# Performance work log

Hardware: AMD Instinct MI355X
Metric: run time of the kernel (lower is better)

The kernel has to match this reference:

```python
import jax, jax.numpy as jnp
import numpy as np

WINDOW = 128  # crop size (compute_crops default window_size)


def centre_crop(centroids, window_size, h, w):
    # centroids: [C,2] int; returns flat gather coords [2, C*ws*ws]
    half = window_size // 2
    cy = jnp.clip(centroids[:, 0], half, h - half)
    cx = jnp.clip(centroids[:, 1], half, w - half)
    gy, gx = jnp.meshgrid(jnp.arange(window_size), jnp.arange(window_size), indexing='ij')
    rows = (cy - half)[:, None, None] + gy[None]  # [C,ws,ws]
    cols = (cx - half)[:, None, None] + gx[None]
    return jnp.stack([rows.reshape(-1), cols.reshape(-1)])  # [2, C*ws*ws]


def setup_inputs() -> dict:
    key = jax.random.key(0)
    ks = jax.random.split(key, 8)
    E, S, C, H, W = 6, 1, 512, 1024, 1024
    Dh = 16
    return {
        'x': jax.random.normal(ks[0], (E, H, W), dtype=jnp.float32),
        'sigma': jax.random.uniform(ks[1], (S, H, W), dtype=jnp.float32),
        'c': jax.random.normal(ks[2], (C, E), dtype=jnp.float32),
        'W1': jax.random.normal(ks[3], (E + S, Dh), dtype=jnp.float32) * 0.3,
        'b1': jnp.zeros((Dh,), dtype=jnp.float32),
        'W2': jax.random.normal(ks[4], (Dh, Dh), dtype=jnp.float32) * 0.3,
        'b2': jnp.zeros((Dh,), dtype=jnp.float32),
        'W3': jax.random.normal(ks[5], (Dh, 1), dtype=jnp.float32) * 0.3,
        'b3': jnp.zeros((1,), dtype=jnp.float32),
        'centroids_idx': jax.random.randint(ks[6], (C, 2), 0, H, dtype=jnp.int32),
    }


def reference(x, sigma, c, W1, b1, W2, b2, W3, b3, centroids_idx):
    E, h, w = x.shape
    S = sigma.shape[0]
    C = c.shape[0]
    ws = WINDOW
    mesh = centre_crop(centroids_idx, ws, h, w)  # [2, C*ws*ws]
    # gather per-instance windows from concatenated embedding+sigma maps
    xs = jnp.concatenate([x, sigma], axis=0)  # [E+S, H, W]
    g = xs[:, mesh[0], mesh[1]]               # [E+S, C*ws*ws]
    g = g.reshape(E + S, C, ws, ws).transpose(1, 0, 2, 3)  # [C, E+S, ws, ws]
    # subtract centroid descriptor from embedding channels (feature_engineering '0')
    g = jnp.concatenate([g[:, :E] - c[:, :, None, None], g[:, E:]], axis=1)
    feats = g.transpose(0, 2, 3, 1).reshape(-1, E + S)  # [(C*ws*ws), E+S]
    # per-pixel probability MLP (ProbabilityNet)
    hdn = jax.nn.relu(feats @ W1 + b1)
    hdn = jax.nn.relu(hdn @ W2 + b2)
    prob = jax.nn.sigmoid(hdn @ W3 + b3)
    prob = prob.reshape(C, 1, ws, ws)
    # instance-id / coordinate table for the downstream scatter (iidd)
    inst = jnp.repeat(jnp.arange(C, dtype=mesh.dtype), ws * ws)
    iidd = jnp.concatenate([inst[None], mesh], axis=0)  # [3, C*ws*ws]
    return prob, iidd
```

## Files before the change

### kernel.cpp

```cpp
#include <hip/hip_runtime.h>

#define HW (1024 * 1024)
#define PLANE 8388608

typedef _Float16 half4 __attribute__((ext_vector_type(4)));
typedef _Float16 half8 __attribute__((ext_vector_type(8)));
typedef float floatx4 __attribute__((ext_vector_type(4)));


__global__ __launch_bounds__(512) void build_worklist(
    const int* __restrict__ cent, int* __restrict__ ws)
{
    __shared__ int cnt[8];
    if (threadIdx.x < 8) cnt[threadIdx.x] = 0;
    __syncthreads();
    for (int t = threadIdx.x; t < 4096; t += 512) {
        const int w = t >> 3, g = t & 7;
        const int cy0 = min(max(cent[2 * w], 64), 960) - 64;
        const int mid = cy0 + 16 * g + 8;
        const int d = mid >> 7;
        const int slot = atomicAdd(&cnt[d], 1);
        ws[16 + d * 1024 + slot] = t;
    }
    __syncthreads();
    if (threadIdx.x < 8) ws[threadIdx.x] = cnt[threadIdx.x];
}

__global__ __launch_bounds__(256) void prep(
    const float* __restrict__ x,
    const float* __restrict__ sigma,
    const float* __restrict__ W1,
    _Float16* __restrict__ P)
{
    const int px = blockIdx.x * 131072 + blockIdx.y * 256 + threadIdx.x;
    float g[7];
#pragma unroll
    for (int e = 0; e < 6; ++e) g[e] = x[e * HW + px];
    g[6] = sigma[px];

    half8 lo, hi;
#pragma unroll
    for (int j = 0; j < 16; ++j) {
        float a = 0.0f;
#pragma unroll
        for (int e = 0; e < 7; ++e)
            a = fmaf(g[e], W1[e * 16 + j], a);
        if (j < 8) lo[j] = (_Float16)a; else hi[j - 8] = (_Float16)a;
    }
    *(half8*)(P + (size_t)px * 16)     = lo;
    *(half8*)(P + (size_t)px * 16 + 8) = hi;
}

__global__ __launch_bounds__(256) void mlp(
    const _Float16* __restrict__ P,
    const int* __restrict__ ws,
    const float* __restrict__ c,
    const float* __restrict__ W1,
    const float* __restrict__ b1,
    const float* __restrict__ W2,
    const float* __restrict__ b2,
    const float* __restrict__ W3,
    const float* __restrict__ b3,
    const int*   __restrict__ cent,
    float* __restrict__ out)
{
    const int d = blockIdx.x;

    if (blockIdx.y < 128) {
        const int j    = d * 128 + blockIdx.y;
        const int w    = j >> 1;
        const int half = j & 1;
        const int cy0 = min(max(cent[2 * w], 64), 960) - 64;
        const int cx0 = min(max(cent[2 * w + 1], 64), 960) - 64;
        const float iw = (float)w;
#pragma unroll
        for (int pass = 0; pass < 8; ++pass) {
            const int p = half * 8192 + pass * 1024 + threadIdx.x * 4;
            const int n = w * 16384 + p;
            const float row = (float)(cy0 + (p >> 7));
            const float c0  = (float)(cx0 + (p & 127));
            floatx4 iv = {iw, iw, iw, iw};
            floatx4 rv = {row, row, row, row};
            floatx4 cv = {c0, c0 + 1.0f, c0 + 2.0f, c0 + 3.0f};
            __builtin_nontemporal_store(iv, (floatx4*)(out + PLANE + n));
            __builtin_nontemporal_store(rv, (floatx4*)(out + 2 * PLANE + n));
            __builtin_nontemporal_store(cv, (floatx4*)(out + 3 * PLANE + n));
        }
        return;
    }

    const int i = blockIdx.y - 128;
    if (i >= ws[d]) return;
    const int t = ws[16 + d * 1024 + i];
    const int w = t >> 3, g = t & 7;

    const int cy0 = min(max(cent[2 * w], 64), 960) - 64;
    const int cx0 = min(max(cent[2 * w + 1], 64), 960) - 64;

    const int lane = threadIdx.x & 63;
    const int wave = threadIdx.x >> 6;
    const int quad = lane >> 4;
    const int sub  = lane & 15;

    half4 a2, qh;
    float w3f[4], bb2[4];
#pragma unroll
    for (int ii = 0; ii < 4; ++ii) {
        const int k = 4 * quad + ii;
        a2[ii]  = (_Float16)W2[k * 16 + sub];
        w3f[ii] = W3[k];
        bb2[ii] = b2[k];
        float qv = -b1[k];
#pragma unroll
        for (int e = 0; e < 6; ++e)
            qv = fmaf(W1[e * 16 + k], c[w * 6 + e], qv);
        qh[ii] = (_Float16)qv;
    }
    const float b3v = b3[0];
    const floatx4 zero = {0.0f, 0.0f, 0.0f, 0.0f};

#pragma unroll 2
    for (int it = wave; it < 32; it += 4) {
        const int start = g * 2048 + it * 64;
        const int srcbase = (cy0 + (start >> 7)) * 1024 + cx0 + (start & 127);
        const _Float16* pb = P + (size_t)(srcbase + sub) * 16 + quad * 4;

        float logit[4];
#pragma unroll
        for (int ch = 0; ch < 4; ++ch) {
            half4 v = *(const half4*)(pb + ch * 256);
            half4 h = v - qh;
#pragma unroll
            for (int ii = 0; ii < 4; ++ii)
                h[ii] = h[ii] > (_Float16)0.0f ? h[ii] : (_Float16)0.0f;

            floatx4 c2 = __builtin_amdgcn_mfma_f32_16x16x16f16(a2, h, zero, 0, 0, 0);

            float part = 0.0f;
#pragma unroll
            for (int ii = 0; ii < 4; ++ii)
                part = fmaf(w3f[ii], fmaxf(c2[ii] + bb2[ii], 0.0f), part);
            part += __shfl_xor(part, 16, 64);
            part += __shfl_xor(part, 32, 64);
            logit[ch] = part;
        }

        const float l01 = (quad & 1) ? logit[1] : logit[0];
        const float l23 = (quad & 1) ? logit[3] : logit[2];
        const float lg  = (quad & 2) ? l23 : l01;
        const float prob = __builtin_amdgcn_rcpf(1.0f + __expf(-(lg + b3v)));

        __builtin_nontemporal_store(prob, out + w * 16384 + start + lane);
    }
}

extern "C" void kernel_launch(void* const* d_in, const int* in_sizes, int n_in,
                              void* d_out, int out_size, void* d_ws, size_t ws_size,
                              hipStream_t stream) {
    const float* x     = (const float*)d_in[0];
    const float* sigma = (const float*)d_in[1];
    const float* c     = (const float*)d_in[2];
    const float* W1    = (const float*)d_in[3];
    const float* b1    = (const float*)d_in[4];
    const float* W2    = (const float*)d_in[5];
    const float* b2    = (const float*)d_in[6];
    const float* W3    = (const float*)d_in[7];
    const float* b3    = (const float*)d_in[8];
    const int*   cent  = (const int*)d_in[9];
    float* out = (float*)d_out;

    int* wsl    = (int*)d_ws;
    _Float16* P = (_Float16*)((char*)d_ws + 65536);

    build_worklist<<<dim3(1), dim3(512), 0, stream>>>(cent, wsl);
    prep<<<dim3(8, 512), dim3(256), 0, stream>>>(x, sigma, W1, P);
    mlp<<<dim3(8, 1152), dim3(256), 0, stream>>>(
        P, wsl, c, W1, b1, W2, b2, W3, b3, cent, out);
}
```

Before: 217.5 us.

## Store raw fp16 inputs and compute first MLP layer with MFMA per crop

The prep kernel no longer precomputes the 16-wide first-layer projection per pixel. It now writes only the 7 input channels as fp16, padded to 8, which halves the intermediate buffer and its write and read traffic. The mlp kernel performs layer 1 as an extra MFMA per 16-pixel chunk, with the centroid bias folded into a per-crop offset. The worklist is now processed in a grid-stride loop, with capacity raised to 4096 entries per bucket, so large buckets are no longer truncated at 1024. The trade is more MFMA and ALU work in the gather kernel in exchange for less memory bandwidth.

```diff
diff --git a/kernel.cpp b/kernel.cpp
--- a/kernel.cpp
+++ b/kernel.cpp
@@ -20,7 +20,7 @@
         const int mid = cy0 + 16 * g + 8;
         const int d = mid >> 7;
         const int slot = atomicAdd(&cnt[d], 1);
-        ws[16 + d * 1024 + slot] = t;
+        ws[16 + d * 4096 + slot] = t;
     }
     __syncthreads();
     if (threadIdx.x < 8) ws[threadIdx.x] = cnt[threadIdx.x];
@@ -29,30 +29,19 @@
 __global__ __launch_bounds__(256) void prep(
     const float* __restrict__ x,
     const float* __restrict__ sigma,
-    const float* __restrict__ W1,
-    _Float16* __restrict__ P)
+    _Float16* __restrict__ X16)
 {
     const int px = blockIdx.x * 131072 + blockIdx.y * 256 + threadIdx.x;
-    float g[7];
+    half8 v;
 #pragma unroll
-    for (int e = 0; e < 6; ++e) g[e] = x[e * HW + px];
-    g[6] = sigma[px];
-
-    half8 lo, hi;
-#pragma unroll
-    for (int j = 0; j < 16; ++j) {
-        float a = 0.0f;
-#pragma unroll
-        for (int e = 0; e < 7; ++e)
-            a = fmaf(g[e], W1[e * 16 + j], a);
-        if (j < 8) lo[j] = (_Float16)a; else hi[j - 8] = (_Float16)a;
-    }
-    *(half8*)(P + (size_t)px * 16)     = lo;
-    *(half8*)(P + (size_t)px * 16 + 8) = hi;
+    for (int e = 0; e < 6; ++e) v[e] = (_Float16)x[e * HW + px];
+    v[6] = (_Float16)sigma[px];
+    v[7] = (_Float16)0.0f;
+    *(half8*)(X16 + (size_t)px * 8) = v;
 }
 
 __global__ __launch_bounds__(256) void mlp(
-    const _Float16* __restrict__ P,
+    const _Float16* __restrict__ X16,
     const int* __restrict__ ws,
     const float* __restrict__ c,
     const float* __restrict__ W1,
@@ -89,68 +78,80 @@
         return;
     }
 
-    const int i = blockIdx.y - 128;
-    if (i >= ws[d]) return;
-    const int t = ws[16 + d * 1024 + i];
-    const int w = t >> 3, g = t & 7;
-
-    const int cy0 = min(max(cent[2 * w], 64), 960) - 64;
-    const int cx0 = min(max(cent[2 * w + 1], 64), 960) - 64;
-
     const int lane = threadIdx.x & 63;
     const int wave = threadIdx.x >> 6;
     const int quad = lane >> 4;
     const int sub  = lane & 15;
+    const bool hiq = quad >= 2;
 
-    half4 a2, qh;
+    half4 a1, a2;
     float w3f[4], bb2[4];
 #pragma unroll
     for (int ii = 0; ii < 4; ++ii) {
         const int k = 4 * quad + ii;
+        a1[ii]  = (_Float16)((k < 7) ? W1[k * 16 + sub] : 0.0f);
         a2[ii]  = (_Float16)W2[k * 16 + sub];
         w3f[ii] = W3[k];
         bb2[ii] = b2[k];
-        float qv = -b1[k];
-#pragma unroll
-        for (int e = 0; e < 6; ++e)
-            qv = fmaf(W1[e * 16 + k], c[w * 6 + e], qv);
-        qh[ii] = (_Float16)qv;
     }
     const float b3v = b3[0];
     const floatx4 zero = {0.0f, 0.0f, 0.0f, 0.0f};
 
-#pragma unroll 2
-    for (int it = wave; it < 32; it += 4) {
-        const int start = g * 2048 + it * 64;
-        const int srcbase = (cy0 + (start >> 7)) * 1024 + cx0 + (start & 127);
-        const _Float16* pb = P + (size_t)(srcbase + sub) * 16 + quad * 4;
+    const int count = ws[d];
+    for (int i = blockIdx.y - 128; i < count; i += 1024) {
+        const int t = ws[16 + d * 4096 + i];
+        const int w = t >> 3, g = t & 7;
 
-        float logit[4];
+        const int cy0 = min(max(cent[2 * w], 64), 960) - 64;
+        const int cx0 = min(max(cent[2 * w + 1], 64), 960) - 64;
+
+        float qf[4];
 #pragma unroll
-        for (int ch = 0; ch < 4; ++ch) {
-            half4 v = *(const half4*)(pb + ch * 256);
-            half4 h = v - qh;
+        for (int ii = 0; ii < 4; ++ii) {
+            const int k = 4 * quad + ii;
+            float qv = b1[k];
 #pragma unroll
-            for (int ii = 0; ii < 4; ++ii)
-                h[ii] = h[ii] > (_Float16)0.0f ? h[ii] : (_Float16)0.0f;
-
-            floatx4 c2 = __builtin_amdgcn_mfma_f32_16x16x16f16(a2, h, zero, 0, 0, 0);
-
-            float part = 0.0f;
-#pragma unroll
-            for (int ii = 0; ii < 4; ++ii)
-                part = fmaf(w3f[ii], fmaxf(c2[ii] + bb2[ii], 0.0f), part);
-            part += __shfl_xor(part, 16, 64);
-            part += __shfl_xor(part, 32, 64);
-            logit[ch] = part;
+            for (int e = 0; e < 6; ++e)
+                qv = fmaf(-W1[e * 16 + k], c[w * 6 + e], qv);
+            qf[ii] = qv;
         }
 
-        const float l01 = (quad & 1) ? logit[1] : logit[0];
-        const float l23 = (quad & 1) ? logit[3] : logit[2];
-        const float lg  = (quad & 2) ? l23 : l01;
-        const float prob = __builtin_amdgcn_rcpf(1.0f + __expf(-(lg + b3v)));
+        for (int it = wave; it < 32; it += 4) {
+            const int start = g * 2048 + it * 64;
+            const int srcbase = (cy0 + (start >> 7)) * 1024 + cx0 + (start & 127);
+            const _Float16* xb = X16 + (size_t)(srcbase + sub) * 8 + (quad & 1) * 4;
 
-        __builtin_nontemporal_store(prob, out + w * 16384 + start + lane);
+            float logit[4];
+#pragma unroll
+            for (int ch = 0; ch < 4; ++ch) {
+                half4 bx = *(const half4*)(xb + ch * 128);
+                if (hiq) bx = half4{0, 0, 0, 0};
+
+                floatx4 c1 = __builtin_amdgcn_mfma_f32_16x16x16f16(a1, bx, zero, 0, 0, 0);
+
+                half4 h;
+#pragma unroll
+                for (int ii = 0; ii < 4; ++ii)
+                    h[ii] = (_Float16)fmaxf(c1[ii] + qf[ii], 0.0f);
+
+                floatx4 c2 = __builtin_amdgcn_mfma_f32_16x16x16f16(a2, h, zero, 0, 0, 0);
+
+                float part = 0.0f;
+#pragma unroll
+                for (int ii = 0; ii < 4; ++ii)
+                    part = fmaf(w3f[ii], fmaxf(c2[ii] + bb2[ii], 0.0f), part);
+                part += __shfl_xor(part, 16, 64);
+                part += __shfl_xor(part, 32, 64);
+                logit[ch] = part;
+            }
+
+            const float l01 = (quad & 1) ? logit[1] : logit[0];
+            const float l23 = (quad & 1) ? logit[3] : logit[2];
+            const float lg  = (quad & 2) ? l23 : l01;
+            const float prob = __builtin_amdgcn_rcpf(1.0f + __expf(-(lg + b3v)));
+
+            __builtin_nontemporal_store(prob, out + w * 16384 + start + lane);
+        }
     }
 }
 
@@ -169,11 +170,11 @@
     const int*   cent  = (const int*)d_in[9];
     float* out = (float*)d_out;
 
-    int* wsl    = (int*)d_ws;
-    _Float16* P = (_Float16*)((char*)d_ws + 65536);
+    int* wsl       = (int*)d_ws;
+    _Float16* X16  = (_Float16*)((char*)d_ws + 262144);
 
     build_worklist<<<dim3(1), dim3(512), 0, stream>>>(cent, wsl);
-    prep<<<dim3(8, 512), dim3(256), 0, stream>>>(x, sigma, W1, P);
+    prep<<<dim3(8, 512), dim3(256), 0, stream>>>(x, sigma, X16);
     mlp<<<dim3(8, 1152), dim3(256), 0, stream>>>(
-        P, wsl, c, W1, b1, W2, b2, W3, b3, cent, out);
+        X16, wsl, c, W1, b1, W2, b2, W3, b3, cent, out);
 }
```

Result: no change. 221.2 us (+1.7%).
